# Performance work log

Hardware: AMD Instinct MI355X
Metric: run time of the kernel (lower is better)

Reference implementation:

```python
import jax, jax.numpy as jnp
import numpy as np

N, E, IN, H, OUT, G = 50000, 800000, 128, 256, 10, 512


def setup_inputs() -> dict:
    key = jax.random.key(0)
    ks = jax.random.split(key, 12)
    def lin(k, fan_in, fan_out):
        s = 1.0 / np.sqrt(fan_in)
        kw, kb = jax.random.split(k)
        W = jax.random.uniform(kw, (fan_in, fan_out), jnp.float32, -s, s)
        b = jax.random.uniform(kb, (fan_out,), jnp.float32, -s, s)
        return W, b
    x = jax.random.normal(ks[0], (N, IN), jnp.float32)
    edge_index = jax.random.randint(ks[1], (2, E), 0, N)
    batch = jnp.sort(jax.random.randint(ks[2], (N,), 0, G))
    W1a, b1a = lin(ks[3], IN, H)
    W1b, b1b = lin(ks[4], H, H)
    W2a, b2a = lin(ks[5], H, H)
    W2b, b2b = lin(ks[6], H, H)
    Wlin, blin = lin(ks[7], H, OUT)
    eps1 = jnp.zeros((), jnp.float32)
    eps2 = jnp.zeros((), jnp.float32)
    return dict(x=x, edge_index=edge_index, batch=batch,
                eps1=eps1, W1a=W1a, b1a=b1a, W1b=W1b, b1b=b1b,
                eps2=eps2, W2a=W2a, b2a=b2a, W2b=W2b, b2b=b2b,
                Wlin=Wlin, blin=blin)


def reference(x, edge_index, batch, eps1, W1a, b1a, W1b, b1b,
              eps2, W2a, b2a, W2b, b2b, Wlin, blin):
    src, dst = edge_index[0], edge_index[1]
    # GINConv 1: h = MLP((1+eps)*x + sum_{j in N(i)} x_j)
    agg = jax.ops.segment_sum(x[src], dst, num_segments=N)  # [N, IN]
    h = (1.0 + eps1) * x + agg
    h = jax.nn.relu(h @ W1a + b1a) @ W1b + b1b              # [N, H]
    h = jax.nn.relu(h)  # (dropout p=0.3 is identity in eval mode)
    # GINConv 2
    agg2 = jax.ops.segment_sum(h[src], dst, num_segments=N)  # [N, H]
    h2 = (1.0 + eps2) * h + agg2
    h2 = jax.nn.relu(h2 @ W2a + b2a) @ W2b + b2b             # [N, H]
    # global mean pool per graph
    psum = jax.ops.segment_sum(h2, batch, num_segments=G)    # [G, H]
    cnt = jax.ops.segment_sum(jnp.ones((N, 1), h2.dtype), batch, num_segments=G)
    pooled = psum / jnp.maximum(cnt, 1.0)
    out = pooled @ Wlin + blin                               # [G, OUT]
    return jax.nn.log_softmax(out, axis=-1)
```

## Files before the change

kernel.cpp:

```cpp
#include <hip/hip_runtime.h>
#include <math.h>
#include <stdint.h>

constexpr int N   = 50000;
constexpr int E   = 800000;
constexpr int IN  = 128;
constexpr int H   = 256;
constexpr int OUT = 10;
constexpr int G   = 512;
constexpr int BSTR = 64;
constexpr int P    = (N + 31) / 32;
constexpr int CAP  = 256;

typedef __bf16 bf16x8 __attribute__((ext_vector_type(8)));
typedef float  f32x4  __attribute__((ext_vector_type(4)));
typedef float  f32x2  __attribute__((ext_vector_type(2)));

__device__ __forceinline__ float blo(unsigned v) { return __uint_as_float(v << 16); }
__device__ __forceinline__ float bhi(unsigned v) { return __uint_as_float(v & 0xffff0000u); }
__device__ __forceinline__ unsigned short f2b(float f) {
  unsigned u = __float_as_uint(f);
  u += 0x7fffu + ((u >> 16) & 1u);
  return (unsigned short)(u >> 16);
}
__device__ __forceinline__ unsigned packb(float lo, float hi) {
  return (unsigned)f2b(lo) | ((unsigned)f2b(hi) << 16);
}
__device__ __forceinline__ unsigned pk_fp8x4(float a, float b, float c, float d) {
  int r = 0;
  r = __builtin_amdgcn_cvt_pk_fp8_f32(a, b, r, false);
  r = __builtin_amdgcn_cvt_pk_fp8_f32(c, d, r, true);
  return (unsigned)r;
}
__device__ __forceinline__ unsigned char fp8_1(float v) {
  return (unsigned char)(__builtin_amdgcn_cvt_pk_fp8_f32(v, v, 0, false) & 0xff);
}


constexpr int EA_BLOCKS  = E / 256;
constexpr int XQ_BLOCKS  = (N * IN / 4) / 256;
constexpr int W1A_BLOCKS = (256 * IN) / 256;
constexpr int WH_BLOCKS  = (256 * H) / 256;

__global__ void prep_kernel(const int* __restrict__ srcp, const int* __restrict__ dstp,
                            int* __restrict__ pcount, unsigned* __restrict__ pbuf,
                            const float* __restrict__ x, unsigned* __restrict__ xq,
                            const float* __restrict__ W1a, unsigned short* __restrict__ Wt1a,
                            const float* __restrict__ W1b, unsigned short* __restrict__ Wt1b,
                            const float* __restrict__ W2a, unsigned short* __restrict__ Wt2a,
                            const float* __restrict__ W2b, unsigned short* __restrict__ Wt2b) {
  int b = blockIdx.x;
  int t = threadIdx.x;
  if (b < EA_BLOCKS) {
    int e = b * 256 + t;
    int d = dstp[e], s = srcp[e];
    int part = d >> 5;
    int slot = ((b & 7) * P) + part;
    int pos = atomicAdd(&pcount[slot], 1);
    if (pos < CAP) pbuf[(size_t)slot * CAP + pos] = ((unsigned)(d & 31) << 16) | (unsigned)s;
    return;
  }
  b -= EA_BLOCKS;
  if (b < XQ_BLOCKS) {
    int id = b * 256 + t;
    float4 v = ((const float4*)x)[id];
    xq[id] = pk_fp8x4(v.x, v.y, v.z, v.w);
    return;
  }
  b -= XQ_BLOCKS;
  if (b < W1A_BLOCKS) {
    int id = b * 256 + t;
    int n = id >> 7, k = id & 127;
    Wt1a[id] = f2b(W1a[k * 256 + n]);
    return;
  }
  b -= W1A_BLOCKS;
  const float* Ws;
  unsigned short* Wd;
  if (b < WH_BLOCKS)            { Ws = W1b; Wd = Wt1b; }
  else if (b < 2 * WH_BLOCKS)   { Ws = W2a; Wd = Wt2a; b -= WH_BLOCKS; }
  else                          { Ws = W2b; Wd = Wt2b; b -= 2 * WH_BLOCKS; }
  int id = b * 256 + t;
  int n = id >> 8, k = id & 255;
  Wd[id] = f2b(Ws[k * 256 + n]);
}


__global__ __launch_bounds__(256) void csr_kernel(const unsigned* __restrict__ pbuf,
                                                  const int* __restrict__ pcount,
                                                  int* __restrict__ deg, int* __restrict__ csre) {
  __shared__ int ldeg[32];
  int p = blockIdx.x;
  int t = threadIdx.x;
  if (t < 32) ldeg[t] = 0;
  __syncthreads();
  for (int x = 0; x < 8; ++x) {
    int slot = x * P + p;
    int cnt = pcount[slot]; if (cnt > CAP) cnt = CAP;
    const unsigned* seg = pbuf + (size_t)slot * CAP;
    for (int k = t; k < cnt; k += 256) {
      unsigned v = seg[k];
      int dl = v >> 16, s = (int)(v & 0xFFFFu);
      int pos = atomicAdd(&ldeg[dl], 1);
      if (pos < BSTR) csre[((size_t)p * 32 + dl) * BSTR + pos] = s;
    }
  }
  __syncthreads();
  if (t < 32) {
    int node = p * 32 + t;
    if (node < N) deg[node] = min(ldeg[t], BSTR);
  }
}


template <int RS>
__global__ __launch_bounds__(64) void agg_pair_kernel(
    const unsigned char* __restrict__ inq,
    const int* __restrict__ deg, const int* __restrict__ csre,
    const float* __restrict__ epsp, unsigned short* __restrict__ out) {
  constexpr int NPAIR = N / 2;
  int bx = blockIdx.x;
  int half = (RS == 256) ? (bx / NPAIR) : 0;
  int pair = (RS == 256) ? (bx - half * NPAIR) : bx;
  int lane = threadIdx.x;
  int hsel = lane >> 5;
  int l = lane & 31;
  int i = pair * 2 + hsel;
  int dg = deg[i]; if (dg > BSTR) dg = BSTR;
  const int* bkt = csre + (size_t)i * BSTR;
  int dgmax = max(dg, __shfl_xor(dg, 32));
  const unsigned char* rowbase = inq + half * 128 + l * 4;
  float a0 = 0.f, a1 = 0.f, a2 = 0.f, a3 = 0.f;
  int hi_j = dg - 1; if (hi_j < 0) hi_j = 0;
  for (int j = 0; j < dgmax; j += 8) {
    unsigned idx[8], v[8];
#pragma unroll
    for (int u = 0; u < 8; ++u) {
      int jc = j + u; if (jc > hi_j) jc = hi_j;
      unsigned raw = (unsigned)bkt[jc];
      idx[u] = raw < (unsigned)N ? raw : 0u;
    }
#pragma unroll
    for (int u = 0; u < 8; ++u) v[u] = *(const unsigned*)(rowbase + (size_t)idx[u] * RS);
#pragma unroll
    for (int u = 0; u < 8; ++u) {
      float s = (j + u < dg) ? 1.f : 0.f;
      f32x2 lo = __builtin_amdgcn_cvt_pk_f32_fp8((int)v[u], false);
      f32x2 hh = __builtin_amdgcn_cvt_pk_f32_fp8((int)v[u], true);
      a0 += s * lo.x; a1 += s * lo.y; a2 += s * hh.x; a3 += s * hh.y;
    }
  }
  float sc = 1.0f + epsp[0];
  unsigned sv = *(const unsigned*)(rowbase + (size_t)i * RS);
  f32x2 slo = __builtin_amdgcn_cvt_pk_f32_fp8((int)sv, false);
  f32x2 shi = __builtin_amdgcn_cvt_pk_f32_fp8((int)sv, true);
  a0 += sc * slo.x; a1 += sc * slo.y; a2 += sc * shi.x; a3 += sc * shi.y;
  unsigned short* orow = out + (size_t)i * RS + half * 128 + l * 4;
  *(uint2*)orow = make_uint2(packb(a0, a1), packb(a2, a3));
}


template <int K, bool RELU, bool OUT8>
__global__ __launch_bounds__(256, 2) void gemm_bf16_kernel(const unsigned short* __restrict__ A,
                                                           const unsigned short* __restrict__ Bt,
                                                           const float* __restrict__ bias,
                                                           void* __restrict__ outv,
                                                           int Nrows) {
  constexpr int M = 256, LDK = 40;
  __shared__ __align__(16) unsigned short As[128 * LDK];
  __shared__ __align__(16) unsigned short Bs[256 * LDK];
  const int tid  = threadIdx.x;
  const int r0   = blockIdx.x * 128;
  const int wave = tid >> 6, lane = tid & 63;
  const int quad = lane >> 4, l15 = lane & 15;
  const int wrow = (wave >> 1) * 64, wcol = (wave & 1) * 64;
  const int srow = tid >> 2;
  const int sk8  = (tid & 3) * 8;

  f32x4 acc[2][4][4];
#pragma unroll
  for (int c = 0; c < 2; ++c)
#pragma unroll
    for (int i = 0; i < 4; ++i)
#pragma unroll
      for (int j = 0; j < 4; ++j) acc[c][i][j] = (f32x4){0.f, 0.f, 0.f, 0.f};

  for (int k0 = 0; k0 < K; k0 += 32) {
    {
      int grow = r0 + srow;
      uint4 v = make_uint4(0u, 0u, 0u, 0u);
      if (grow < Nrows) v = *(const uint4*)(A + (size_t)grow * K + k0 + sk8);
      *(uint4*)(As + srow * LDK + sk8) = v;
      grow = r0 + srow + 64;
      uint4 w = make_uint4(0u, 0u, 0u, 0u);
      if (grow < Nrows) w = *(const uint4*)(A + (size_t)grow * K + k0 + sk8);
      *(uint4*)(As + (srow + 64) * LDK + sk8) = w;
#pragma unroll
      for (int sgm = 0; sgm < 4; ++sgm) {
        int col = srow + sgm * 64;
        *(uint4*)(Bs + col * LDK + sk8) = *(const uint4*)(Bt + (size_t)col * K + k0 + sk8);
      }
    }
    __syncthreads();
    bf16x8 af[4];
#pragma unroll
    for (int mt = 0; mt < 4; ++mt)
      af[mt] = *(const bf16x8*)(As + (wrow + mt * 16 + l15) * LDK + quad * 8);
#pragma unroll
    for (int ch = 0; ch < 2; ++ch) {
      bf16x8 bfr[4];
#pragma unroll
      for (int nt = 0; nt < 4; ++nt)
        bfr[nt] = *(const bf16x8*)(Bs + (ch * 128 + wcol + nt * 16 + l15) * LDK + quad * 8);
#pragma unroll
      for (int mt = 0; mt < 4; ++mt)
#pragma unroll
        for (int nt = 0; nt < 4; ++nt)
          acc[ch][mt][nt] =
              __builtin_amdgcn_mfma_f32_16x16x32_bf16(af[mt], bfr[nt], acc[ch][mt][nt], 0, 0, 0);
    }
    __syncthreads();
  }

#pragma unroll
  for (int ch = 0; ch < 2; ++ch) {
    float bv[4];
#pragma unroll
    for (int nt = 0; nt < 4; ++nt) bv[nt] = bias[ch * 128 + wcol + nt * 16 + l15];
#pragma unroll
    for (int mt = 0; mt < 4; ++mt) {
      int gr0 = r0 + wrow + mt * 16 + quad * 4;
#pragma unroll
      for (int i = 0; i < 4; ++i) {
        int grow = gr0 + i;
        if (grow >= Nrows) continue;
#pragma unroll
        for (int nt = 0; nt < 4; ++nt) {
          float v = acc[ch][mt][nt][i] + bv[nt];
          if (RELU) v = fmaxf(v, 0.f);
          int col = ch * 128 + wcol + nt * 16 + l15;
          if (OUT8) ((unsigned char*)outv)[(size_t)grow * M + col] = fp8_1(v);
          else      ((unsigned short*)outv)[(size_t)grow * M + col] = f2b(v);
        }
      }
    }
  }
}


__global__ __launch_bounds__(128) void pool_final_kernel(const unsigned short* __restrict__ h2,
                                                         const int* __restrict__ batch,
                                                         const float* __restrict__ Wlin,
                                                         const float* __restrict__ blin,
                                                         float* __restrict__ out) {
  __shared__ float sp[H];
  __shared__ float logits[OUT];
  int g = blockIdx.x;
  int t = threadIdx.x;
  int lo = 0, hi = N;
  while (lo < hi) { int m = (lo + hi) >> 1; if (batch[m] < g) lo = m + 1; else hi = m; }
  int s = lo;
  lo = 0; hi = N;
  while (lo < hi) { int m = (lo + hi) >> 1; if (batch[m] < g + 1) lo = m + 1; else hi = m; }
  int e = lo;
  float a0 = 0.f, a1 = 0.f;
  const unsigned* base = (const unsigned*)h2;
  int n = s;
  for (; n + 4 <= e; n += 4) {
    unsigned v0 = base[(size_t)(n + 0) * (H / 2) + t];
    unsigned v1 = base[(size_t)(n + 1) * (H / 2) + t];
    unsigned v2 = base[(size_t)(n + 2) * (H / 2) + t];
    unsigned v3 = base[(size_t)(n + 3) * (H / 2) + t];
    a0 += blo(v0) + blo(v1) + blo(v2) + blo(v3);
    a1 += bhi(v0) + bhi(v1) + bhi(v2) + bhi(v3);
  }
  for (; n < e; ++n) {
    unsigned v = base[(size_t)n * (H / 2) + t];
    a0 += blo(v); a1 += bhi(v);
  }
  float inv = 1.0f / fmaxf((float)(e - s), 1.0f);
  sp[2 * t]     = a0 * inv;
  sp[2 * t + 1] = a1 * inv;
  __syncthreads();
  if (t < OUT) {
    float acc = blin[t];
    for (int k = 0; k < H; ++k) acc = fmaf(sp[k], Wlin[k * OUT + t], acc);
    logits[t] = acc;
  }
  __syncthreads();
  if (t == 0) {
    float m = -INFINITY;
    for (int j = 0; j < OUT; ++j) m = fmaxf(m, logits[j]);
    float ssum = 0.f;
    for (int j = 0; j < OUT; ++j) ssum += expf(logits[j] - m);
    float ls = logf(ssum);
    for (int j = 0; j < OUT; ++j) out[(size_t)g * OUT + j] = logits[j] - m - ls;
  }
}


static inline char* align_up(char* p, size_t a) {
  return (char*)(((uintptr_t)p + a - 1) & ~(a - 1));
}

extern "C" void kernel_launch(void* const* d_in, const int* in_sizes, int n_in,
                              void* d_out, int out_size, void* d_ws, size_t ws_size,
                              hipStream_t stream) {
  const float* x    = (const float*)d_in[0];
  const int*   ei   = (const int*)d_in[1];
  const int*   srcp = ei;
  const int*   dstp = ei + E;
  const int*   batch = (const int*)d_in[2];
  const float* eps1 = (const float*)d_in[3];
  const float* W1a  = (const float*)d_in[4];
  const float* b1a  = (const float*)d_in[5];
  const float* W1b  = (const float*)d_in[6];
  const float* b1b  = (const float*)d_in[7];
  const float* eps2 = (const float*)d_in[8];
  const float* W2a  = (const float*)d_in[9];
  const float* b2a  = (const float*)d_in[10];
  const float* W2b  = (const float*)d_in[11];
  const float* b2b  = (const float*)d_in[12];
  const float* Wlin = (const float*)d_in[13];
  const float* blin = (const float*)d_in[14];
  float* outp = (float*)d_out;

  char* p = (char*)d_ws;
  int* pcount = (int*)p;             p = align_up(p + (size_t)8 * P * 4, 256);
  unsigned* pbuf = (unsigned*)p;     p = align_up(p + (size_t)8 * P * CAP * 4, 256);
  int* deg  = (int*)p;               p = align_up(p + (size_t)N * 4, 256);
  int* csre = (int*)p;               p = align_up(p + (size_t)N * BSTR * 4, 256);
  unsigned* xq = (unsigned*)p;       p = align_up(p + (size_t)N * IN, 256);
  unsigned char* h1q = (unsigned char*)p;  p = align_up(p + (size_t)N * H, 256);
  unsigned short* B1 = (unsigned short*)p; p = align_up(p + (size_t)N * IN * 2, 256);
  unsigned short* B2 = (unsigned short*)p; p = align_up(p + (size_t)N * H * 2, 256);
  unsigned short* B3 = (unsigned short*)p; p = align_up(p + (size_t)N * H * 2, 256);
  unsigned short* Wt1a = (unsigned short*)p;  p = align_up(p + (size_t)H * IN * 2, 256);
  unsigned short* Wt1b = (unsigned short*)p;  p = align_up(p + (size_t)H * H * 2, 256);
  unsigned short* Wt2a = (unsigned short*)p;  p = align_up(p + (size_t)H * H * 2, 256);
  unsigned short* Wt2b = (unsigned short*)p;  p = align_up(p + (size_t)H * H * 2, 256);

  hipMemsetAsync(pcount, 0, (size_t)8 * P * 4, stream);

  prep_kernel<<<EA_BLOCKS + XQ_BLOCKS + W1A_BLOCKS + 3 * WH_BLOCKS, 256, 0, stream>>>(
      srcp, dstp, pcount, pbuf, x, xq, W1a, Wt1a, W1b, Wt1b, W2a, Wt2a, W2b, Wt2b);

  csr_kernel<<<P, 256, 0, stream>>>(pbuf, pcount, deg, csre);

  const int ggrid = (N + 127) / 128;

  agg_pair_kernel<IN><<<N / 2, 64, 0, stream>>>((const unsigned char*)xq, deg, csre, eps1, B1);
  gemm_bf16_kernel<IN, true, false><<<ggrid, 256, 0, stream>>>(B1, Wt1a, b1a, B2, N);
  gemm_bf16_kernel<H, true, true><<<ggrid, 256, 0, stream>>>(B2, Wt1b, b1b, h1q, N);

  agg_pair_kernel<H><<<N, 64, 0, stream>>>(h1q, deg, csre, eps2, B3);
  gemm_bf16_kernel<H, true, false><<<ggrid, 256, 0, stream>>>(B3, Wt2a, b2a, B2, N);
  gemm_bf16_kernel<H, false, false><<<ggrid, 256, 0, stream>>>(B2, Wt2b, b2b, B3, N);

  pool_final_kernel<<<G, 128, 0, stream>>>(B3, batch, Wlin, blin, outp);
}
```

Baseline: 289.2 us.

## Bucket edges per block with shared-memory counters and prefix-scan CSR build

Edge bucketing now gives each block a fixed chunk of 4096 edges and counts into shared-memory cursors for 391 partitions of 128 nodes each. Each block writes into its own private segment, so the global atomics and the memset of the partition counters are no longer needed. The CSR kernel runs a block-wide prefix scan over the per-block counts and binary-searches to gather the edges of each partition. This cuts global atomic contention and the number of CSR blocks. The cost is a fixed segment capacity of 48 per block and partition, so edges are silently dropped if a segment overflows, plus extra scan and search work.

```diff
diff --git a/kernel.cpp b/kernel.cpp
--- a/kernel.cpp
+++ b/kernel.cpp
@@ -9,8 +9,11 @@
 constexpr int OUT = 10;
 constexpr int G   = 512;
 constexpr int BSTR = 64;
-constexpr int P    = (N + 31) / 32;
-constexpr int CAP  = 256;
+
+constexpr int NPART  = 391;
+constexpr int SEGCAP = 48;
+constexpr int EPB    = 4096;
+constexpr int AB     = (E + EPB - 1) / EPB;
 
 typedef __bf16 bf16x8 __attribute__((ext_vector_type(8)));
 typedef float  f32x4  __attribute__((ext_vector_type(4)));
@@ -37,30 +40,48 @@
 }
 
 
-constexpr int EA_BLOCKS  = E / 256;
 constexpr int XQ_BLOCKS  = (N * IN / 4) / 256;
 constexpr int W1A_BLOCKS = (256 * IN) / 256;
 constexpr int WH_BLOCKS  = (256 * H) / 256;
 
-__global__ void prep_kernel(const int* __restrict__ srcp, const int* __restrict__ dstp,
-                            int* __restrict__ pcount, unsigned* __restrict__ pbuf,
-                            const float* __restrict__ x, unsigned* __restrict__ xq,
-                            const float* __restrict__ W1a, unsigned short* __restrict__ Wt1a,
-                            const float* __restrict__ W1b, unsigned short* __restrict__ Wt1b,
-                            const float* __restrict__ W2a, unsigned short* __restrict__ Wt2a,
-                            const float* __restrict__ W2b, unsigned short* __restrict__ Wt2b) {
+__global__ __launch_bounds__(256) void prep_kernel(
+    const int* __restrict__ srcp, const int* __restrict__ dstp,
+    unsigned* __restrict__ pbuf, int* __restrict__ pcnt,
+    const float* __restrict__ x, unsigned* __restrict__ xq,
+    const float* __restrict__ W1a, unsigned short* __restrict__ Wt1a,
+    const float* __restrict__ W1b, unsigned short* __restrict__ Wt1b,
+    const float* __restrict__ W2a, unsigned short* __restrict__ Wt2a,
+    const float* __restrict__ W2b, unsigned short* __restrict__ Wt2b) {
+  __shared__ int lcur[NPART];
   int b = blockIdx.x;
   int t = threadIdx.x;
-  if (b < EA_BLOCKS) {
-    int e = b * 256 + t;
-    int d = dstp[e], s = srcp[e];
-    int part = d >> 5;
-    int slot = ((b & 7) * P) + part;
-    int pos = atomicAdd(&pcount[slot], 1);
-    if (pos < CAP) pbuf[(size_t)slot * CAP + pos] = ((unsigned)(d & 31) << 16) | (unsigned)s;
+  if (b < AB) {
+    for (int j = t; j < NPART; j += 256) lcur[j] = 0;
+    __syncthreads();
+    const int e0 = b * EPB;
+#pragma unroll
+    for (int r = 0; r < EPB / 1024; ++r) {
+      int base = e0 + (r * 256 + t) * 4;
+      if (base < E) {
+        int4 d4 = *(const int4*)(dstp + base);
+        int4 s4 = *(const int4*)(srcp + base);
+        int dd[4] = {d4.x, d4.y, d4.z, d4.w};
+        int ss[4] = {s4.x, s4.y, s4.z, s4.w};
+#pragma unroll
+        for (int u = 0; u < 4; ++u) {
+          int part = dd[u] >> 7, dl = dd[u] & 127;
+          int pos = atomicAdd(&lcur[part], 1);
+          if (pos < SEGCAP)
+            pbuf[((size_t)part * AB + b) * SEGCAP + pos] =
+                ((unsigned)dl << 16) | (unsigned)ss[u];
+        }
+      }
+    }
+    __syncthreads();
+    for (int j = t; j < NPART; j += 256) pcnt[b * NPART + j] = min(lcur[j], SEGCAP);
     return;
   }
-  b -= EA_BLOCKS;
+  b -= AB;
   if (b < XQ_BLOCKS) {
     int id = b * 256 + t;
     float4 v = ((const float4*)x)[id];
@@ -87,27 +108,37 @@
 
 
 __global__ __launch_bounds__(256) void csr_kernel(const unsigned* __restrict__ pbuf,
-                                                  const int* __restrict__ pcount,
+                                                  const int* __restrict__ pcnt,
                                                   int* __restrict__ deg, int* __restrict__ csre) {
-  __shared__ int ldeg[32];
+  __shared__ int sa[256], sb[256];
+  __shared__ int ldeg[128];
   int p = blockIdx.x;
   int t = threadIdx.x;
-  if (t < 32) ldeg[t] = 0;
+  if (t < 128) ldeg[t] = 0;
+  sa[t] = (t < AB) ? pcnt[t * NPART + p] : 0;
   __syncthreads();
-  for (int x = 0; x < 8; ++x) {
-    int slot = x * P + p;
-    int cnt = pcount[slot]; if (cnt > CAP) cnt = CAP;
-    const unsigned* seg = pbuf + (size_t)slot * CAP;
-    for (int k = t; k < cnt; k += 256) {
-      unsigned v = seg[k];
-      int dl = v >> 16, s = (int)(v & 0xFFFFu);
-      int pos = atomicAdd(&ldeg[dl], 1);
-      if (pos < BSTR) csre[((size_t)p * 32 + dl) * BSTR + pos] = s;
-    }
+  int* cur = sa; int* nxt = sb;
+#pragma unroll
+  for (int off = 1; off < 256; off <<= 1) {
+    nxt[t] = cur[t] + ((t >= off) ? cur[t - off] : 0);
+    __syncthreads();
+    int* tmp = cur; cur = nxt; nxt = tmp;
+  }
+  int T = cur[255];
+  const unsigned* seg = pbuf + (size_t)p * AB * SEGCAP;
+  for (int f = t; f < T; f += 256) {
+    int lo = 0, hi = AB - 1;
+    while (lo < hi) { int m = (lo + hi) >> 1; if (cur[m] > f) hi = m; else lo = m + 1; }
+    int bb = lo;
+    int excl = bb ? cur[bb - 1] : 0;
+    unsigned v = seg[(size_t)bb * SEGCAP + (f - excl)];
+    int dl = (int)(v >> 16), s = (int)(v & 0xFFFFu);
+    int pos = atomicAdd(&ldeg[dl], 1);
+    if (pos < BSTR) csre[(((size_t)p << 7) + dl) * BSTR + pos] = s;
   }
   __syncthreads();
-  if (t < 32) {
-    int node = p * 32 + t;
+  if (t < 128) {
+    int node = (p << 7) + t;
     if (node < N) deg[node] = min(ldeg[t], BSTR);
   }
 }
@@ -326,10 +357,10 @@
   float* outp = (float*)d_out;
 
   char* p = (char*)d_ws;
-  int* pcount = (int*)p;             p = align_up(p + (size_t)8 * P * 4, 256);
-  unsigned* pbuf = (unsigned*)p;     p = align_up(p + (size_t)8 * P * CAP * 4, 256);
+  unsigned* pbuf = (unsigned*)p;     p = align_up(p + (size_t)NPART * AB * SEGCAP * 4, 256);
+  int* pcnt = (int*)p;               p = align_up(p + (size_t)AB * NPART * 4, 256);
   int* deg  = (int*)p;               p = align_up(p + (size_t)N * 4, 256);
-  int* csre = (int*)p;               p = align_up(p + (size_t)N * BSTR * 4, 256);
+  int* csre = (int*)p;               p = align_up(p + (size_t)NPART * 128 * BSTR * 4, 256);
   unsigned* xq = (unsigned*)p;       p = align_up(p + (size_t)N * IN, 256);
   unsigned char* h1q = (unsigned char*)p;  p = align_up(p + (size_t)N * H, 256);
   unsigned short* B1 = (unsigned short*)p; p = align_up(p + (size_t)N * IN * 2, 256);
@@ -340,12 +371,10 @@
   unsigned short* Wt2a = (unsigned short*)p;  p = align_up(p + (size_t)H * H * 2, 256);
   unsigned short* Wt2b = (unsigned short*)p;  p = align_up(p + (size_t)H * H * 2, 256);
 
-  hipMemsetAsync(pcount, 0, (size_t)8 * P * 4, stream);
-
-  prep_kernel<<<EA_BLOCKS + XQ_BLOCKS + W1A_BLOCKS + 3 * WH_BLOCKS, 256, 0, stream>>>(
-      srcp, dstp, pcount, pbuf, x, xq, W1a, Wt1a, W1b, Wt1b, W2a, Wt2a, W2b, Wt2b);
-
-  csr_kernel<<<P, 256, 0, stream>>>(pbuf, pcount, deg, csre);
+  prep_kernel<<<AB + XQ_BLOCKS + W1A_BLOCKS + 3 * WH_BLOCKS, 256, 0, stream>>>(
+      srcp, dstp, pbuf, pcnt, x, xq, W1a, Wt1a, W1b, Wt1b, W2a, Wt2a, W2b, Wt2b);
+
+  csr_kernel<<<NPART, 256, 0, stream>>>(pbuf, pcnt, deg, csre);
 
   const int ggrid = (N + 127) / 128;
 
```

Result: faster. 262.5 us (-9.2%).
